# Kernel optimization log

Measured on AMD Instinct MI355X. Metric: run time of the kernel, lower is better.

## Reference

```python
import jax, jax.numpy as jnp
import numpy as np

B, C, H, W = 4, 64, 128, 128
Q = 65536
OUT_SIZE = 256  # output image side -> cell = 2/OUT_SIZE
HIDDEN = 256
D_IN = C + 2 + 2  # feat + rel_coord + rel_cell


def setup_inputs() -> dict:
    key = jax.random.key(0)
    ks = jax.random.split(key, 8)
    feat = jax.random.normal(ks[0], (B, C, H, W), dtype=jnp.float32)
    coord = jax.random.uniform(ks[1], (B, Q, 2), dtype=jnp.float32, minval=-1.0, maxval=1.0)
    cell = jnp.full((B, Q, 2), 2.0 / OUT_SIZE, dtype=jnp.float32)

    def lin(k, din, dout):
        return jax.random.normal(k, (din, dout), dtype=jnp.float32) * (1.0 / np.sqrt(din))

    w0 = lin(ks[2], D_IN, HIDDEN)
    w1 = lin(ks[3], HIDDEN, HIDDEN)
    w2 = lin(ks[4], HIDDEN, HIDDEN)
    w3 = lin(ks[5], HIDDEN, HIDDEN)
    w4 = lin(ks[6], HIDDEN, 3)
    z = lambda d: jnp.zeros((d,), dtype=jnp.float32)
    return {"feat": feat, "coord": coord, "cell": cell,
            "w0": w0, "b0": z(HIDDEN), "w1": w1, "b1": z(HIDDEN),
            "w2": w2, "b2": z(HIDDEN), "w3": w3, "b3": z(HIDDEN),
            "w4": w4, "b4": z(3)}


def _liif(feat, coord, cell, ws, bs):
    b, c, h, w = feat.shape
    eps = 1e-6
    rx, ry = 1.0 / h, 1.0 / w  # 2/h/2, 2/w/2
    # local ensemble shifts, loop order vx outer, vy inner: (-1,-1),(-1,1),(1,-1),(1,1)
    shifts = jnp.array([[-rx, -ry], [-rx, ry], [rx, -ry], [rx, ry]], dtype=feat.dtype) + eps
    feat_flat = feat.reshape(b, c, h * w)
    cell_scale = jnp.array([h, w], dtype=feat.dtype)
    rel_cell = cell * cell_scale  # same for all branches

    def branch(shift):
        cshift = jnp.clip(coord + shift, -1.0 + eps, 1.0 - eps)
        # nearest grid_sample, align_corners=False: idx = floor((x+1)*size/2), clamped
        iy = jnp.clip(jnp.floor((cshift[..., 0] + 1.0) * (h * 0.5)), 0.0, h - 1.0).astype(jnp.int32)
        ix = jnp.clip(jnp.floor((cshift[..., 1] + 1.0) * (w * 0.5)), 0.0, w - 1.0).astype(jnp.int32)
        idx = iy * w + ix  # [B, Q]
        q_feat = jnp.take_along_axis(feat_flat, idx[:, None, :], axis=2)  # [B, C, Q]
        q_feat = q_feat.transpose(0, 2, 1)  # [B, Q, C]
        # feat_coord at the gathered pixel (make_coord values)
        qc0 = -1.0 + (2.0 * iy.astype(feat.dtype) + 1.0) / h
        qc1 = -1.0 + (2.0 * ix.astype(feat.dtype) + 1.0) / w
        rel0 = (coord[..., 0] - qc0) * h
        rel1 = (coord[..., 1] - qc1) * w
        inp = jnp.concatenate([q_feat, rel0[..., None], rel1[..., None], rel_cell], axis=-1)
        x = inp
        for wi, bi in zip(ws[:-1], bs[:-1]):
            x = jax.nn.relu(x @ wi + bi)
        pred = x @ ws[-1] + bs[-1]  # [B, Q, 3]
        area = jnp.abs(rel0 * rel1) + 1e-9  # [B, Q]
        return pred, area

    preds, areas = jax.vmap(branch)(shifts)  # [4,B,Q,3], [4,B,Q]
    tot = areas.sum(axis=0)
    # diagonal weight swap: 0<->3, 1<->2  == reverse
    wgt = areas[::-1] / tot
    return (preds * wgt[..., None]).sum(axis=0)  # [B, Q, 3]


def reference(feat, coord, cell, w0, b0, w1, b1, w2, b2, w3, b3, w4, b4):
    ws = [w0, w1, w2, w3, w4]
    bs = [b0, b1, b2, b3, b4]
    return _liif(feat, coord, cell, ws, bs)
```

## Files before the change

### kernel.cpp

```cpp
#include <hip/hip_runtime.h>
#include <cstdint>

typedef __bf16 bf16x8 __attribute__((ext_vector_type(8)));
typedef float f32x4 __attribute__((ext_vector_type(4)));
typedef unsigned int u32x4 __attribute__((ext_vector_type(4)));
typedef unsigned int u32x2 __attribute__((ext_vector_type(2)));
typedef unsigned short u16;
typedef unsigned int u32;

#define HH 128
#define WW 128
#define CC 64
#define QQ 65536
#define BB 4

#define RS 264

#define L0_OFF 0
#define L1_OFF 24576
#define L2_OFF 90112
#define L3_OFF 155648
#define W4_OFF 221184
#define FEATT_BYTE_OFF 524288u

__global__ void pack_weights(const float* __restrict__ w0,
                             const float* __restrict__ w1,
                             const float* __restrict__ w2,
                             const float* __restrict__ w3,
                             const float* __restrict__ w4,
                             u16* __restrict__ ws_us) {
    int bid = blockIdx.x;
    int lane = threadIdx.x;
    int tile, nk, off, Ksrc, Ncols, NT;
    const float* w;
    if (bid < 48)       { tile = bid;       nk = 3; off = L0_OFF; w = w0; Ksrc = 68;  Ncols = 256; NT = 16; }
    else if (bid < 176) { tile = bid - 48;  nk = 8; off = L1_OFF; w = w1; Ksrc = 256; Ncols = 256; NT = 16; }
    else if (bid < 304) { tile = bid - 176; nk = 8; off = L2_OFF; w = w2; Ksrc = 256; Ncols = 256; NT = 16; }
    else if (bid < 432) { tile = bid - 304; nk = 8; off = L3_OFF; w = w3; Ksrc = 256; Ncols = 256; NT = 16; }
    else                { tile = bid - 432; nk = 8; off = W4_OFF; w = w4; Ksrc = 256; Ncols = 3;   NT = 1;  }
    int kt = tile % nk;
    int nt = tile / nk;
    int n = nt * 16 + (lane & 15);
    int kbase = kt * 32 + (lane >> 4) * 8;
    unsigned int d[4];
    for (int i = 0; i < 4; ++i) {
        unsigned int lo, hi;
        {
            int k = kbase + 2 * i;
            float x = (k < Ksrc && n < Ncols) ? w[k * Ncols + n] : 0.0f;
            __bf16 hb = (__bf16)x;
            lo = (unsigned int)__builtin_bit_cast(u16, hb);
        }
        {
            int k = kbase + 2 * i + 1;
            float x = (k < Ksrc && n < Ncols) ? w[k * Ncols + n] : 0.0f;
            __bf16 hb = (__bf16)x;
            hi = (unsigned int)__builtin_bit_cast(u16, hb);
        }
        d[i] = lo | (hi << 16);
    }
    u32x4 pk = { d[0], d[1], d[2], d[3] };
    int dst = off + (kt * NT + nt) * 512 + lane * 8;
    *reinterpret_cast<u32x4*>(ws_us + dst) = pk;
}

__global__ void prep_featT(const float* __restrict__ feat, u16* __restrict__ featT) {
    __shared__ u16 tile[128 * 66];
    int bid = blockIdx.x;
    int b = bid >> 7, y = bid & 127;
    for (int idx = threadIdx.x; idx < CC * WW; idx += 256) {
        int c = idx >> 7, x = idx & 127;
        float v = feat[(((b * CC + c) * HH + y) * WW) + x];
        __bf16 hb = (__bf16)v;
        tile[x * 66 + c] = __builtin_bit_cast(u16, hb);
    }
    __syncthreads();
    for (int idx = threadIdx.x; idx < 2048; idx += 256) {
        int x = idx >> 4, c4 = (idx & 15) * 4;
        const u16* src = tile + x * 66 + c4;
        u32x2 d;
        d[0] = (unsigned int)src[0] | ((unsigned int)src[1] << 16);
        d[1] = (unsigned int)src[2] | ((unsigned int)src[3] << 16);
        *reinterpret_cast<u32x2*>(featT + ((b * HH + y) * WW + x) * CC + c4) = d;
    }
}

template <int NK>
__device__ __forceinline__ void gemm_layer(const u16* __restrict__ src,
                                           u16* __restrict__ dst,
                                           const u32x4* __restrict__ wbase,
                                           const float* __restrict__ bias,
                                           int wave, int lane,
                                           const u32x4 wpre[2],
                                           u32x4 wnxt[2],
                                           const u32x4* __restrict__ wnb,
                                           int vnxt) {
    f32x4 acc[2][4] = {};
    const int l15 = lane & 15;
    const int qd = lane >> 4;
    const int voff = wave * 128 + lane;
    const u16* xb = src + l15 * RS + qd * 8;
    u16* db = dst + l15 * RS + wave * 32 + qd * 4;

    u32x4 wq[2][2];
    wq[0][0] = wpre[0];
    wq[0][1] = wpre[1];

    bf16x8 xc[4];
#pragma unroll
    for (int st = 0; st < 4; ++st)
        xc[st] = __builtin_bit_cast(bf16x8,
            *reinterpret_cast<const u32x4*>(xb + st * 16 * RS));

#pragma unroll
    for (int kt = 0; kt < NK; ++kt) {
        if (kt + 1 < NK) {
            const u32x4* wn = wbase + (kt + 1) * 1024;
#pragma unroll
            for (int fi = 0; fi < 2; ++fi)
                wq[(kt + 1) & 1][fi] = wn[voff + fi * 64];
        }
#pragma unroll
        for (int st = 0; st < 4; ++st) {
#pragma unroll
            for (int fi = 0; fi < 2; ++fi)
                acc[fi][st] = __builtin_amdgcn_mfma_f32_16x16x32_bf16(
                    __builtin_bit_cast(bf16x8, wq[kt & 1][fi]), xc[st],
                    acc[fi][st], 0, 0, 0);
            if (kt + 1 < NK)
                xc[st] = __builtin_bit_cast(bf16x8,
                    *reinterpret_cast<const u32x4*>(xb + st * 16 * RS + (kt + 1) * 32));
        }
    }

#pragma unroll
    for (int fi = 0; fi < 2; ++fi) wnxt[fi] = wnb[vnxt + fi * 64];

#pragma unroll
    for (int fi = 0; fi < 2; ++fi) {
        int fbase = wave * 32 + fi * 16 + qd * 4;
        f32x4 bv = *reinterpret_cast<const f32x4*>(bias + fbase);
#pragma unroll
        for (int st = 0; st < 4; ++st) {
            float v0 = fmaxf(acc[fi][st][0] + bv[0], 0.0f);
            float v1 = fmaxf(acc[fi][st][1] + bv[1], 0.0f);
            float v2 = fmaxf(acc[fi][st][2] + bv[2], 0.0f);
            float v3 = fmaxf(acc[fi][st][3] + bv[3], 0.0f);
            __bf16 h0 = (__bf16)v0, h1 = (__bf16)v1, h2 = (__bf16)v2, h3 = (__bf16)v3;
            u32x2 d;
            d[0] = (u32)__builtin_bit_cast(u16, h0) | ((u32)__builtin_bit_cast(u16, h1) << 16);
            d[1] = (u32)__builtin_bit_cast(u16, h2) | ((u32)__builtin_bit_cast(u16, h3) << 16);
            *reinterpret_cast<u32x2*>(db + st * 16 * RS + fi * 16) = d;
        }
    }
}

__global__ __launch_bounds__(512, 4) void liif_main(
    const float* __restrict__ coord, const float* __restrict__ cell,
    const float* __restrict__ b0, const float* __restrict__ b1,
    const float* __restrict__ b2, const float* __restrict__ b3,
    const float* __restrict__ b4,
    const u16* __restrict__ wpack, const u16* __restrict__ featT,
    float* __restrict__ out) {
    __shared__ u16 bufA[64 * RS];
    __shared__ u16 bufB[64 * RS];
    __shared__ float areasLDS[64];

    const int t = threadIdx.x;
    const int wave = t >> 6, lane = t & 63;
    const int row = t >> 3, p = t & 7;

    const int bq = blockIdx.x * 16 + (row >> 2);
    const int v = row & 3;
    const int b = bq >> 16;
    const float c0 = coord[bq * 2 + 0];
    const float c1 = coord[bq * 2 + 1];
    const float rc0 = cell[bq * 2 + 0] * 128.0f;
    const float rc1 = cell[bq * 2 + 1] * 128.0f;
    const float eps = 1e-6f;
    const float sx = ((v & 2) ? 0.0078125f : -0.0078125f) + eps;
    const float sy = ((v & 1) ? 0.0078125f : -0.0078125f) + eps;
    float cs0 = fminf(fmaxf(c0 + sx, -1.0f + eps), 1.0f - eps);
    float cs1 = fminf(fmaxf(c1 + sy, -1.0f + eps), 1.0f - eps);
    float fy = fminf(fmaxf(floorf((cs0 + 1.0f) * 64.0f), 0.0f), 127.0f);
    float fx = fminf(fmaxf(floorf((cs1 + 1.0f) * 64.0f), 0.0f), 127.0f);
    int iy = (int)fy, ix = (int)fx;
    float qc0 = -1.0f + (2.0f * fy + 1.0f) * 0.0078125f;
    float qc1 = -1.0f + (2.0f * fx + 1.0f) * 0.0078125f;
    float rel0 = (c0 - qc0) * 128.0f;
    float rel1 = (c1 - qc1) * 128.0f;
    float area = fabsf(rel0 * rel1) + 1e-9f;

    {
        const u16* fr = featT + (((b * HH + iy) * WW + ix) * CC) + p * 8;
        u32x4 f0 = *reinterpret_cast<const u32x4*>(fr);
        u16* sb = bufA + row * RS;
        *reinterpret_cast<u32x4*>(sb + p * 8) = f0;
        if (p < 4) {
            u32x4 e = { 0u, 0u, 0u, 0u };
            if (p == 0) {
                __bf16 h0 = (__bf16)rel0, h1 = (__bf16)rel1, h2 = (__bf16)rc0, h3 = (__bf16)rc1;
                e[0] = (u32)__builtin_bit_cast(u16, h0) | ((u32)__builtin_bit_cast(u16, h1) << 16);
                e[1] = (u32)__builtin_bit_cast(u16, h2) | ((u32)__builtin_bit_cast(u16, h3) << 16);
                areasLDS[row] = area;
            }
            *reinterpret_cast<u32x4*>(sb + 64 + p * 8) = e;
        }
    }

    const u32x4* wp = reinterpret_cast<const u32x4*>(wpack);
    const u32x4* wp0 = wp + (L0_OFF / 8);
    const u32x4* wp1 = wp + (L1_OFF / 8);
    const u32x4* wp2 = wp + (L2_OFF / 8);
    const u32x4* wp3 = wp + (L3_OFF / 8);
    const u32x4* wp4 = wp + (W4_OFF / 8);
    const int voff = wave * 128 + lane;

    u32x4 wA[2], wB[2];
    wA[0] = wp0[voff];
    wA[1] = wp0[voff + 64];
    __syncthreads();
    gemm_layer<3>(bufA, bufB, wp0, b0, wave, lane, wA, wB, wp1, voff);
    __syncthreads();
    gemm_layer<8>(bufB, bufA, wp1, b1, wave, lane, wB, wA, wp2, voff);
    __syncthreads();
    gemm_layer<8>(bufA, bufB, wp2, b2, wave, lane, wA, wB, wp3, voff);
    __syncthreads();
    gemm_layer<8>(bufB, bufA, wp3, b3, wave, lane, wB, wA, wp4, lane);
    u32x4 w4r[6];
#pragma unroll
    for (int i = 0; i < 6; ++i) w4r[i] = wp4[(i + 2) * 64 + lane];
    __syncthreads();

    if (wave < 4) {
        const int l15 = lane & 15;
        const int qd = lane >> 4;
        const u16* xb = bufA + (wave * 16 + l15) * RS + qd * 8;
        f32x4 accf = {};
#pragma unroll
        for (int kt = 0; kt < 2; ++kt) {
            bf16x8 x = __builtin_bit_cast(bf16x8,
                *reinterpret_cast<const u32x4*>(xb + kt * 32));
            accf = __builtin_amdgcn_mfma_f32_16x16x32_bf16(
                __builtin_bit_cast(bf16x8, wA[kt]), x, accf, 0, 0, 0);
        }
#pragma unroll
        for (int kt = 2; kt < 8; ++kt) {
            bf16x8 x = __builtin_bit_cast(bf16x8,
                *reinterpret_cast<const u32x4*>(xb + kt * 32));
            accf = __builtin_amdgcn_mfma_f32_16x16x32_bf16(
                __builtin_bit_cast(bf16x8, w4r[kt - 2]), x, accf, 0, 0, 0);
        }
        float a = areasLDS[wave * 16 + l15];
        float a1 = a + __shfl_xor(a, 1);
        float asum = a1 + __shfl_xor(a1, 2);
        float aopp = __shfl_xor(a, 3);
        float wgt = aopp / asum;
        float o0 = (accf[0] + b4[0]) * wgt;
        float o1 = (accf[1] + b4[1]) * wgt;
        float o2 = (accf[2] + b4[2]) * wgt;
        o0 += __shfl_xor(o0, 1); o0 += __shfl_xor(o0, 2);
        o1 += __shfl_xor(o1, 1); o1 += __shfl_xor(o1, 2);
        o2 += __shfl_xor(o2, 1); o2 += __shfl_xor(o2, 2);

        if (qd == 0 && (l15 & 3) == 0) {
            int obq = blockIdx.x * 16 + wave * 4 + (l15 >> 2);
            out[obq * 3 + 0] = o0;
            out[obq * 3 + 1] = o1;
            out[obq * 3 + 2] = o2;
        }
    }
}

extern "C" void kernel_launch(void* const* d_in, const int* in_sizes, int n_in,
                              void* d_out, int out_size, void* d_ws, size_t ws_size,
                              hipStream_t stream) {
    const float* feat  = (const float*)d_in[0];
    const float* coord = (const float*)d_in[1];
    const float* cell  = (const float*)d_in[2];
    const float* w0 = (const float*)d_in[3];
    const float* b0 = (const float*)d_in[4];
    const float* w1 = (const float*)d_in[5];
    const float* b1 = (const float*)d_in[6];
    const float* w2 = (const float*)d_in[7];
    const float* b2 = (const float*)d_in[8];
    const float* w3 = (const float*)d_in[9];
    const float* b3 = (const float*)d_in[10];
    const float* w4 = (const float*)d_in[11];
    const float* b4 = (const float*)d_in[12];

    u16* ws_us = (u16*)d_ws;
    u16* featT = (u16*)((char*)d_ws + FEATT_BYTE_OFF);

    hipLaunchKernelGGL(pack_weights, dim3(440), dim3(64), 0, stream,
                       w0, w1, w2, w3, w4, ws_us);
    hipLaunchKernelGGL(prep_featT, dim3(BB * HH), dim3(256), 0, stream, feat, featT);
    hipLaunchKernelGGL(liif_main, dim3((BB * QQ) / 16), dim3(512), 0, stream,
                       coord, cell, b0, b1, b2, b3, b4, ws_us, featT,
                       (float*)d_out);
}
```

Baseline: 537.0 us.

## Switch hidden-layer GEMMs to 32x32x16 MFMA with repacked weight tiles

Hidden MLP layers now use 32x32x16 bf16 MFMA instructions instead of 16x16x32. Each wave computes a 32-row by 64-column tile (two accumulators), and the weight pack kernel emits 16x32 k-by-n tiles to match. Weights and activations are prefetched three k-steps ahead through a rotating register ring. The larger MFMA shape raises operand reuse per LDS and global load, at the cost of more accumulator registers and a changed wave-to-tile mapping that must line up with the unchanged final layer.

```diff
diff --git a/kernel.cpp b/kernel.cpp
--- a/kernel.cpp
+++ b/kernel.cpp
@@ -3,6 +3,7 @@
 
 typedef __bf16 bf16x8 __attribute__((ext_vector_type(8)));
 typedef float f32x4 __attribute__((ext_vector_type(4)));
+typedef float f32x16 __attribute__((ext_vector_type(16)));
 typedef unsigned int u32x4 __attribute__((ext_vector_type(4)));
 typedef unsigned int u32x2 __attribute__((ext_vector_type(2)));
 typedef unsigned short u16;
@@ -31,37 +32,61 @@
                              u16* __restrict__ ws_us) {
     int bid = blockIdx.x;
     int lane = threadIdx.x;
-    int tile, nk, off, Ksrc, Ncols, NT;
-    const float* w;
-    if (bid < 48)       { tile = bid;       nk = 3; off = L0_OFF; w = w0; Ksrc = 68;  Ncols = 256; NT = 16; }
-    else if (bid < 176) { tile = bid - 48;  nk = 8; off = L1_OFF; w = w1; Ksrc = 256; Ncols = 256; NT = 16; }
-    else if (bid < 304) { tile = bid - 176; nk = 8; off = L2_OFF; w = w2; Ksrc = 256; Ncols = 256; NT = 16; }
-    else if (bid < 432) { tile = bid - 304; nk = 8; off = L3_OFF; w = w3; Ksrc = 256; Ncols = 256; NT = 16; }
-    else                { tile = bid - 432; nk = 8; off = W4_OFF; w = w4; Ksrc = 256; Ncols = 3;   NT = 1;  }
-    int kt = tile % nk;
-    int nt = tile / nk;
-    int n = nt * 16 + (lane & 15);
-    int kbase = kt * 32 + (lane >> 4) * 8;
-    unsigned int d[4];
-    for (int i = 0; i < 4; ++i) {
-        unsigned int lo, hi;
-        {
-            int k = kbase + 2 * i;
-            float x = (k < Ksrc && n < Ncols) ? w[k * Ncols + n] : 0.0f;
-            __bf16 hb = (__bf16)x;
-            lo = (unsigned int)__builtin_bit_cast(u16, hb);
-        }
-        {
-            int k = kbase + 2 * i + 1;
-            float x = (k < Ksrc && n < Ncols) ? w[k * Ncols + n] : 0.0f;
-            __bf16 hb = (__bf16)x;
-            hi = (unsigned int)__builtin_bit_cast(u16, hb);
-        }
-        d[i] = lo | (hi << 16);
-    }
-    u32x4 pk = { d[0], d[1], d[2], d[3] };
-    int dst = off + (kt * NT + nt) * 512 + lane * 8;
-    *reinterpret_cast<u32x4*>(ws_us + dst) = pk;
+    if (bid < 432) {
+        int tile, off, Ksrc;
+        const float* w;
+        if (bid < 48)       { tile = bid;       off = L0_OFF; w = w0; Ksrc = 68;  }
+        else if (bid < 176) { tile = bid - 48;  off = L1_OFF; w = w1; Ksrc = 256; }
+        else if (bid < 304) { tile = bid - 176; off = L2_OFF; w = w2; Ksrc = 256; }
+        else                { tile = bid - 304; off = L3_OFF; w = w3; Ksrc = 256; }
+        int kt = tile >> 3, nt = tile & 7;
+        int n = nt * 32 + (lane & 31);
+        int kbase = kt * 16 + (lane >> 5) * 8;
+        unsigned int d[4];
+        for (int i = 0; i < 4; ++i) {
+            unsigned int lo, hi;
+            {
+                int k = kbase + 2 * i;
+                float x = (k < Ksrc) ? w[k * 256 + n] : 0.0f;
+                __bf16 hb = (__bf16)x;
+                lo = (unsigned int)__builtin_bit_cast(u16, hb);
+            }
+            {
+                int k = kbase + 2 * i + 1;
+                float x = (k < Ksrc) ? w[k * 256 + n] : 0.0f;
+                __bf16 hb = (__bf16)x;
+                hi = (unsigned int)__builtin_bit_cast(u16, hb);
+            }
+            d[i] = lo | (hi << 16);
+        }
+        u32x4 pk = { d[0], d[1], d[2], d[3] };
+        int dst = off + tile * 512 + lane * 8;
+        *reinterpret_cast<u32x4*>(ws_us + dst) = pk;
+    } else {
+        int kt = bid - 432;
+        int n = lane & 15;
+        int kbase = kt * 32 + (lane >> 4) * 8;
+        unsigned int d[4];
+        for (int i = 0; i < 4; ++i) {
+            unsigned int lo, hi;
+            {
+                int k = kbase + 2 * i;
+                float x = (n < 3) ? w4[k * 3 + n] : 0.0f;
+                __bf16 hb = (__bf16)x;
+                lo = (unsigned int)__builtin_bit_cast(u16, hb);
+            }
+            {
+                int k = kbase + 2 * i + 1;
+                float x = (n < 3) ? w4[k * 3 + n] : 0.0f;
+                __bf16 hb = (__bf16)x;
+                hi = (unsigned int)__builtin_bit_cast(u16, hb);
+            }
+            d[i] = lo | (hi << 16);
+        }
+        u32x4 pk = { d[0], d[1], d[2], d[3] };
+        int dst = W4_OFF + kt * 512 + lane * 8;
+        *reinterpret_cast<u32x4*>(ws_us + dst) = pk;
+    }
 }
 
 __global__ void prep_featT(const float* __restrict__ feat, u16* __restrict__ featT) {
@@ -86,71 +111,69 @@
 }
 
 template <int NK>
-__device__ __forceinline__ void gemm_layer(const u16* __restrict__ src,
-                                           u16* __restrict__ dst,
-                                           const u32x4* __restrict__ wbase,
-                                           const float* __restrict__ bias,
-                                           int wave, int lane,
-                                           const u32x4 wpre[2],
-                                           u32x4 wnxt[2],
-                                           const u32x4* __restrict__ wnb,
-                                           int vnxt) {
-    f32x4 acc[2][4] = {};
-    const int l15 = lane & 15;
-    const int qd = lane >> 4;
-    const int voff = wave * 128 + lane;
-    const u16* xb = src + l15 * RS + qd * 8;
-    u16* db = dst + l15 * RS + wave * 32 + qd * 4;
-
-    u32x4 wq[2][2];
+__device__ __forceinline__ void gemm_layer32(const u16* __restrict__ src,
+                                             u16* __restrict__ dst,
+                                             const u32x4* __restrict__ wbase,
+                                             const float* __restrict__ bias,
+                                             int wave, int lane,
+                                             const u32x4 wpre[2],
+                                             u32x4 wnxt[2],
+                                             const u32x4* __restrict__ wnb,
+                                             int vnxt) {
+    f32x16 acc[2] = {};
+    const int l31 = lane & 31;
+    const int kh = lane >> 5;
+    const int st = wave >> 2;
+    const int np = wave & 3;
+    const int voff = np * 128 + lane;
+    const u16* xb = src + (st * 32 + l31) * RS + kh * 8;
+    u16* db = dst + (st * 32 + l31) * RS + np * 64 + kh * 4;
+
+    u32x4 wq[3][2];
     wq[0][0] = wpre[0];
     wq[0][1] = wpre[1];
-
-    bf16x8 xc[4];
-#pragma unroll
-    for (int st = 0; st < 4; ++st)
-        xc[st] = __builtin_bit_cast(bf16x8,
-            *reinterpret_cast<const u32x4*>(xb + st * 16 * RS));
+    if (NK > 1) { wq[1][0] = wbase[512 + voff];  wq[1][1] = wbase[512 + voff + 64]; }
+    if (NK > 2) { wq[2][0] = wbase[1024 + voff]; wq[2][1] = wbase[1024 + voff + 64]; }
+
+    u32x4 xq[3];
+    xq[0] = *reinterpret_cast<const u32x4*>(xb);
+    if (NK > 1) xq[1] = *reinterpret_cast<const u32x4*>(xb + 16);
+    if (NK > 2) xq[2] = *reinterpret_cast<const u32x4*>(xb + 32);
 
 #pragma unroll
     for (int kt = 0; kt < NK; ++kt) {
-        if (kt + 1 < NK) {
-            const u32x4* wn = wbase + (kt + 1) * 1024;
-#pragma unroll
-            for (int fi = 0; fi < 2; ++fi)
-                wq[(kt + 1) & 1][fi] = wn[voff + fi * 64];
-        }
-#pragma unroll
-        for (int st = 0; st < 4; ++st) {
-#pragma unroll
-            for (int fi = 0; fi < 2; ++fi)
-                acc[fi][st] = __builtin_amdgcn_mfma_f32_16x16x32_bf16(
-                    __builtin_bit_cast(bf16x8, wq[kt & 1][fi]), xc[st],
-                    acc[fi][st], 0, 0, 0);
-            if (kt + 1 < NK)
-                xc[st] = __builtin_bit_cast(bf16x8,
-                    *reinterpret_cast<const u32x4*>(xb + st * 16 * RS + (kt + 1) * 32));
-        }
-    }
-
-#pragma unroll
-    for (int fi = 0; fi < 2; ++fi) wnxt[fi] = wnb[vnxt + fi * 64];
+        acc[0] = __builtin_amdgcn_mfma_f32_32x32x16_bf16(
+            __builtin_bit_cast(bf16x8, wq[kt % 3][0]),
+            __builtin_bit_cast(bf16x8, xq[kt % 3]), acc[0], 0, 0, 0);
+        acc[1] = __builtin_amdgcn_mfma_f32_32x32x16_bf16(
+            __builtin_bit_cast(bf16x8, wq[kt % 3][1]),
+            __builtin_bit_cast(bf16x8, xq[kt % 3]), acc[1], 0, 0, 0);
+        if (kt + 3 < NK) {
+            const u32x4* wn = wbase + (kt + 3) * 512;
+            wq[kt % 3][0] = wn[voff];
+            wq[kt % 3][1] = wn[voff + 64];
+            xq[kt % 3] = *reinterpret_cast<const u32x4*>(xb + (kt + 3) * 16);
+        }
+    }
+
+    wnxt[0] = wnb[vnxt];
+    wnxt[1] = wnb[vnxt + 64];
 
 #pragma unroll
     for (int fi = 0; fi < 2; ++fi) {
-        int fbase = wave * 32 + fi * 16 + qd * 4;
-        f32x4 bv = *reinterpret_cast<const f32x4*>(bias + fbase);
-#pragma unroll
-        for (int st = 0; st < 4; ++st) {
-            float v0 = fmaxf(acc[fi][st][0] + bv[0], 0.0f);
-            float v1 = fmaxf(acc[fi][st][1] + bv[1], 0.0f);
-            float v2 = fmaxf(acc[fi][st][2] + bv[2], 0.0f);
-            float v3 = fmaxf(acc[fi][st][3] + bv[3], 0.0f);
+        int fbase = (np * 2 + fi) * 32 + kh * 4;
+#pragma unroll
+        for (int g = 0; g < 4; ++g) {
+            f32x4 bv = *reinterpret_cast<const f32x4*>(bias + fbase + g * 8);
+            float v0 = fmaxf(acc[fi][g * 4 + 0] + bv[0], 0.0f);
+            float v1 = fmaxf(acc[fi][g * 4 + 1] + bv[1], 0.0f);
+            float v2 = fmaxf(acc[fi][g * 4 + 2] + bv[2], 0.0f);
+            float v3 = fmaxf(acc[fi][g * 4 + 3] + bv[3], 0.0f);
             __bf16 h0 = (__bf16)v0, h1 = (__bf16)v1, h2 = (__bf16)v2, h3 = (__bf16)v3;
             u32x2 d;
             d[0] = (u32)__builtin_bit_cast(u16, h0) | ((u32)__builtin_bit_cast(u16, h1) << 16);
             d[1] = (u32)__builtin_bit_cast(u16, h2) | ((u32)__builtin_bit_cast(u16, h3) << 16);
-            *reinterpret_cast<u32x2*>(db + st * 16 * RS + fi * 16) = d;
+            *reinterpret_cast<u32x2*>(db + fi * 32 + g * 8) = d;
         }
     }
 }
@@ -214,19 +237,19 @@
     const u32x4* wp2 = wp + (L2_OFF / 8);
     const u32x4* wp3 = wp + (L3_OFF / 8);
     const u32x4* wp4 = wp + (W4_OFF / 8);
-    const int voff = wave * 128 + lane;
+    const int voff = (wave & 3) * 128 + lane;
 
     u32x4 wA[2], wB[2];
     wA[0] = wp0[voff];
     wA[1] = wp0[voff + 64];
     __syncthreads();
-    gemm_layer<3>(bufA, bufB, wp0, b0, wave, lane, wA, wB, wp1, voff);
-    __syncthreads();
-    gemm_layer<8>(bufB, bufA, wp1, b1, wave, lane, wB, wA, wp2, voff);
-    __syncthreads();
-    gemm_layer<8>(bufA, bufB, wp2, b2, wave, lane, wA, wB, wp3, voff);
-    __syncthreads();
-    gemm_layer<8>(bufB, bufA, wp3, b3, wave, lane, wB, wA, wp4, lane);
+    gemm_layer32<6>(bufA, bufB, wp0, b0, wave, lane, wA, wB, wp1, voff);
+    __syncthreads();
+    gemm_layer32<16>(bufB, bufA, wp1, b1, wave, lane, wB, wA, wp2, voff);
+    __syncthreads();
+    gemm_layer32<16>(bufA, bufB, wp2, b2, wave, lane, wA, wB, wp3, voff);
+    __syncthreads();
+    gemm_layer32<16>(bufB, bufA, wp3, b3, wave, lane, wB, wA, wp4, lane);
     u32x4 w4r[6];
 #pragma unroll
     for (int i = 0; i < 6; ++i) w4r[i] = wp4[(i + 2) * 64 + lane];
```

Measured after the change: 692.0 us. 28.9% more time.

## Retile MLP GEMM waves to 2x4 split with deeper weight/activation prefetch

Applied to the files above, without the earlier changes.

Changes the per-wave work split in each hidden layer from each wave owning 32 output features across all 64 rows to a 2x4 grid. Each wave now owns 64 features by 32 rows, so it holds 4 weight fragments and 2 activation fragments per k-step. It also prefetches both weights and activations two k-steps ahead, and the final layer's preloaded weight fragments are adjusted to match. The aim is a better balance between global weight loads and LDS activation reads per MFMA, and more latency hiding. The cost is more registers under a 512-thread, 4-block launch bound, and the global weight traffic per wave doubles.

```diff
diff --git a/kernel.cpp b/kernel.cpp
--- a/kernel.cpp
+++ b/kernel.cpp
@@ -91,57 +91,67 @@
                                            const u32x4* __restrict__ wbase,
                                            const float* __restrict__ bias,
                                            int wave, int lane,
-                                           const u32x4 wpre[2],
-                                           u32x4 wnxt[2],
+                                           const u32x4 wpre[4],
+                                           u32x4 wnxt[4],
                                            const u32x4* __restrict__ wnb,
                                            int vnxt) {
-    f32x4 acc[2][4] = {};
+    f32x4 acc[4][2] = {};
     const int l15 = lane & 15;
     const int qd = lane >> 4;
-    const int voff = wave * 128 + lane;
-    const u16* xb = src + l15 * RS + qd * 8;
-    u16* db = dst + l15 * RS + wave * 32 + qd * 4;
-
-    u32x4 wq[2][2];
-    wq[0][0] = wpre[0];
-    wq[0][1] = wpre[1];
-
-    bf16x8 xc[4];
-#pragma unroll
-    for (int st = 0; st < 4; ++st)
-        xc[st] = __builtin_bit_cast(bf16x8,
-            *reinterpret_cast<const u32x4*>(xb + st * 16 * RS));
+    const int sp = wave >> 2;
+    const int ng = wave & 3;
+    const int voff = ng * 256 + lane;
+    const u16* xb = src + (sp * 32 + l15) * RS + qd * 8;
+    u16* db = dst + (sp * 32 + l15) * RS + ng * 64 + qd * 4;
+
+    u32x4 wq[2][4];
+#pragma unroll
+    for (int fi = 0; fi < 4; ++fi) wq[0][fi] = wpre[fi];
+    if (NK > 1) {
+#pragma unroll
+        for (int fi = 0; fi < 4; ++fi) wq[1][fi] = wbase[1024 + voff + fi * 64];
+    }
+
+    u32x4 xq[2][2];
+#pragma unroll
+    for (int st = 0; st < 2; ++st)
+        xq[0][st] = *reinterpret_cast<const u32x4*>(xb + st * 16 * RS);
+    if (NK > 1) {
+#pragma unroll
+        for (int st = 0; st < 2; ++st)
+            xq[1][st] = *reinterpret_cast<const u32x4*>(xb + st * 16 * RS + 32);
+    }
 
 #pragma unroll
     for (int kt = 0; kt < NK; ++kt) {
-        if (kt + 1 < NK) {
-            const u32x4* wn = wbase + (kt + 1) * 1024;
-#pragma unroll
-            for (int fi = 0; fi < 2; ++fi)
-                wq[(kt + 1) & 1][fi] = wn[voff + fi * 64];
-        }
-#pragma unroll
-        for (int st = 0; st < 4; ++st) {
-#pragma unroll
-            for (int fi = 0; fi < 2; ++fi)
+#pragma unroll
+        for (int fi = 0; fi < 4; ++fi)
+#pragma unroll
+            for (int st = 0; st < 2; ++st)
                 acc[fi][st] = __builtin_amdgcn_mfma_f32_16x16x32_bf16(
-                    __builtin_bit_cast(bf16x8, wq[kt & 1][fi]), xc[st],
+                    __builtin_bit_cast(bf16x8, wq[kt & 1][fi]),
+                    __builtin_bit_cast(bf16x8, xq[kt & 1][st]),
                     acc[fi][st], 0, 0, 0);
-            if (kt + 1 < NK)
-                xc[st] = __builtin_bit_cast(bf16x8,
-                    *reinterpret_cast<const u32x4*>(xb + st * 16 * RS + (kt + 1) * 32));
-        }
-    }
-
-#pragma unroll
-    for (int fi = 0; fi < 2; ++fi) wnxt[fi] = wnb[vnxt + fi * 64];
-
-#pragma unroll
-    for (int fi = 0; fi < 2; ++fi) {
-        int fbase = wave * 32 + fi * 16 + qd * 4;
+        if (kt + 2 < NK) {
+            const u32x4* wn = wbase + (kt + 2) * 1024;
+#pragma unroll
+            for (int fi = 0; fi < 4; ++fi) wq[kt & 1][fi] = wn[voff + fi * 64];
+#pragma unroll
+            for (int st = 0; st < 2; ++st)
+                xq[kt & 1][st] = *reinterpret_cast<const u32x4*>(
+                    xb + st * 16 * RS + (kt + 2) * 32);
+        }
+    }
+
+#pragma unroll
+    for (int fi = 0; fi < 4; ++fi) wnxt[fi] = wnb[vnxt + fi * 64];
+
+#pragma unroll
+    for (int fi = 0; fi < 4; ++fi) {
+        int fbase = (ng * 4 + fi) * 16 + qd * 4;
         f32x4 bv = *reinterpret_cast<const f32x4*>(bias + fbase);
 #pragma unroll
-        for (int st = 0; st < 4; ++st) {
+        for (int st = 0; st < 2; ++st) {
             float v0 = fmaxf(acc[fi][st][0] + bv[0], 0.0f);
             float v1 = fmaxf(acc[fi][st][1] + bv[1], 0.0f);
             float v2 = fmaxf(acc[fi][st][2] + bv[2], 0.0f);
@@ -214,11 +224,11 @@
     const u32x4* wp2 = wp + (L2_OFF / 8);
     const u32x4* wp3 = wp + (L3_OFF / 8);
     const u32x4* wp4 = wp + (W4_OFF / 8);
-    const int voff = wave * 128 + lane;
-
-    u32x4 wA[2], wB[2];
-    wA[0] = wp0[voff];
-    wA[1] = wp0[voff + 64];
+    const int voff = (wave & 3) * 256 + lane;
+
+    u32x4 wA[4], wB[4];
+#pragma unroll
+    for (int fi = 0; fi < 4; ++fi) wA[fi] = wp0[voff + fi * 64];
     __syncthreads();
     gemm_layer<3>(bufA, bufB, wp0, b0, wave, lane, wA, wB, wp1, voff);
     __syncthreads();
@@ -227,9 +237,9 @@
     gemm_layer<8>(bufA, bufB, wp2, b2, wave, lane, wA, wB, wp3, voff);
     __syncthreads();
     gemm_layer<8>(bufB, bufA, wp3, b3, wave, lane, wB, wA, wp4, lane);
-    u32x4 w4r[6];
-#pragma unroll
-    for (int i = 0; i < 6; ++i) w4r[i] = wp4[(i + 2) * 64 + lane];
+    u32x4 w4r[4];
+#pragma unroll
+    for (int i = 0; i < 4; ++i) w4r[i] = wp4[(i + 4) * 64 + lane];
     __syncthreads();
 
     if (wave < 4) {
@@ -238,18 +248,18 @@
         const u16* xb = bufA + (wave * 16 + l15) * RS + qd * 8;
         f32x4 accf = {};
 #pragma unroll
-        for (int kt = 0; kt < 2; ++kt) {
+        for (int kt = 0; kt < 4; ++kt) {
             bf16x8 x = __builtin_bit_cast(bf16x8,
                 *reinterpret_cast<const u32x4*>(xb + kt * 32));
             accf = __builtin_amdgcn_mfma_f32_16x16x32_bf16(
                 __builtin_bit_cast(bf16x8, wA[kt]), x, accf, 0, 0, 0);
         }
 #pragma unroll
-        for (int kt = 2; kt < 8; ++kt) {
+        for (int kt = 4; kt < 8; ++kt) {
             bf16x8 x = __builtin_bit_cast(bf16x8,
                 *reinterpret_cast<const u32x4*>(xb + kt * 32));
             accf = __builtin_amdgcn_mfma_f32_16x16x32_bf16(
-                __builtin_bit_cast(bf16x8, w4r[kt - 2]), x, accf, 0, 0, 0);
+                __builtin_bit_cast(bf16x8, w4r[kt - 4]), x, accf, 0, 0, 0);
         }
         float a = areasLDS[wave * 16 + l15];
         float a1 = a + __shfl_xor(a, 1);
```

Measured after the change: 629.4 us. 17.2% more time.
